# Kernel tuning notes

Hardware: AMD Instinct MI355X
Metric: run time of the kernel (lower is better)

## Reference

```python
import jax, jax.numpy as jnp
import numpy as np

# Module constants (from GaussRenderer.__init__ with image 128x128)
H = 128
W = 128
TS = 64          # TILE_SIZE
P_MAX = 2048
WHITE_BKGD = True
TH, TW = H // TS, W // TS
NT = TH * TW     # num_tiles


def _tile_grids():
    th, tw = jnp.meshgrid(jnp.arange(TH), jnp.arange(TW), indexing='ij')
    h_mins = (th * TS).reshape(-1).astype(jnp.float32)   # [NT]
    w_mins = (tw * TS).reshape(-1).astype(jnp.float32)   # [NT]
    lx = jnp.arange(TS, dtype=jnp.float32)
    xx, yy = jnp.meshgrid(lx, lx, indexing='xy')         # xx[i,j]=j, yy[i,j]=i
    local = jnp.stack([xx, yy], axis=-1).reshape(TS * TS, 2)
    # tile_coords[t, p] = (x, y) global pixel coordinate
    coords = local[None, :, :] + jnp.stack([w_mins, h_mins], axis=-1)[:, None, :]
    return h_mins, w_mins, coords


def setup_inputs() -> dict:
    key = jax.random.key(0)
    k1, k2, k3, k4, k5 = jax.random.split(key, 5)
    N = 100000
    means2D = jax.random.uniform(k1, (N, 2), dtype=jnp.float32) * jnp.array([float(W), float(H)], dtype=jnp.float32)
    A = jax.random.normal(k2, (N, 2, 2), dtype=jnp.float32) * 2.0
    cov2d = A @ jnp.swapaxes(A, 1, 2) + 0.5 * jnp.eye(2, dtype=jnp.float32)  # SPD
    color = jax.random.uniform(k3, (N, 3), dtype=jnp.float32)
    opacity = jax.random.uniform(k4, (N, 1), dtype=jnp.float32)
    depths = jax.random.uniform(k5, (N,), dtype=jnp.float32) * 10.0 + 0.2
    return {"means2D": means2D, "cov2d": cov2d, "color": color, "opacity": opacity, "depths": depths}


def _render(means2D, cov2d, color, opacity, depths):
    h_mins, w_mins, tile_coords = _tile_grids()
    h_maxs = h_mins + (TS - 1.0)
    w_maxs = w_mins + (TS - 1.0)

    # --- get_radius / get_rect (torch.no_grad -> stop_gradient) ---
    c = jax.lax.stop_gradient(cov2d)
    det = c[:, 0, 0] * c[:, 1, 1] - c[:, 0, 1] * c[:, 1, 0]
    mid = 0.5 * (c[:, 0, 0] + c[:, 1, 1])
    s = jnp.sqrt(jnp.clip(mid ** 2 - det, 0.1, None))
    radii = 3.0 * jnp.ceil(jnp.sqrt(jnp.maximum(mid + s, mid - s)))  # [N]
    m = jax.lax.stop_gradient(means2D)
    rmin = m - radii[:, None]
    rmax = m + radii[:, None]
    rmin = jnp.stack([jnp.clip(rmin[:, 0], 0.0, W - 1.0), jnp.clip(rmin[:, 1], 0.0, H - 1.0)], axis=-1)
    rmax = jnp.stack([jnp.clip(rmax[:, 0], 0.0, W - 1.0), jnp.clip(rmax[:, 1], 0.0, H - 1.0)], axis=-1)

    # --- tile/gaussian overlap test ---
    ov_x = jnp.minimum(rmax[None, :, 0], w_maxs[:, None]) > jnp.maximum(rmin[None, :, 0], w_mins[:, None])
    ov_y = jnp.minimum(rmax[None, :, 1], h_maxs[:, None]) > jnp.maximum(rmin[None, :, 1], h_mins[:, None])
    overlap = ov_x & ov_y                                   # [NT, N]

    # --- per-tile depth sort, keep front-most P_MAX ---
    FAR = jnp.float32(1e10)
    d_tiled = jnp.where(overlap, depths[None, :], FAR)      # [NT, N]
    idx = jnp.argsort(d_tiled, axis=1)[:, :P_MAX]           # [NT, P]
    sd = jnp.take_along_axis(d_tiled, idx, axis=1)          # sorted depths
    valid = (sd < 1e9).astype(means2D.dtype)                # [NT, P]

    sm = means2D[idx]          # [NT, P, 2]
    sc = cov2d[idx]            # [NT, P, 2, 2]
    so = opacity[idx][..., 0]  # [NT, P]
    scol = color[idx]          # [NT, P, 3]

    # --- conic (inverse 2x2 covariance) ---
    a_ = sc[..., 0, 0]; b_ = sc[..., 0, 1]; c2_ = sc[..., 1, 0]; d_ = sc[..., 1, 1]
    inv_det = 1.0 / jnp.clip(a_ * d_ - b_ * c2_, 1e-6, None)
    c00 = d_ * inv_det; c01 = -b_ * inv_det; c10 = -c2_ * inv_det; c11 = a_ * inv_det

    # --- per-pixel gaussian weights: [NT, TS*TS, P] ---
    dx0 = tile_coords[:, :, None, 0] - sm[:, None, :, 0]
    dx1 = tile_coords[:, :, None, 1] - sm[:, None, :, 1]
    gw = jnp.exp(-0.5 * (dx0 * dx0 * c00[:, None, :] + dx1 * dx1 * c11[:, None, :]
                         + dx0 * dx1 * (c01 + c10)[:, None, :]))

    # --- front-to-back alpha compositing ---
    alpha = jnp.minimum(gw * so[:, None, :], 0.99) * valid[:, None, :]
    T = jnp.cumprod(jnp.concatenate([jnp.ones_like(alpha[:, :, :1]), 1.0 - alpha[:, :, :-1]], axis=2), axis=2)
    w = alpha * T                                           # [NT, TS*TS, P]
    acc = w.sum(axis=2)                                     # [NT, TS*TS]
    tcol = jnp.einsum('tpn,tnc->tpc', w, scol)              # [NT, TS*TS, 3]
    if WHITE_BKGD:
        tcol = tcol + (1.0 - acc)[..., None]
    tdep = (w * sd[:, None, :]).sum(axis=2)

    # --- untile ---
    render_color = tcol.reshape(TH, TW, TS, TS, 3).transpose(0, 2, 1, 3, 4).reshape(H, W, 3)
    render_depth = tdep.reshape(TH, TW, TS, TS).transpose(0, 2, 1, 3).reshape(H, W, 1)
    render_alpha = acc.reshape(TH, TW, TS, TS).transpose(0, 2, 1, 3).reshape(H, W, 1)
    return render_color, render_depth, render_alpha


def reference(means2D, cov2d, color, opacity, depths):
    return _render(means2D, cov2d, color, opacity, depths)
```

## Files before the change

kernel.cpp:

```cpp
#include <hip/hip_runtime.h>

#define IMG 128
#define TSZ 64
#define NTILES 4
#define PMAX 2048
#define NHIST 4096
#define CAP 64
#define NCHUNK 16
#define CHUNK 128
#define QCH 32
#define NPIX 4096
#define NPSEG 16
#define PLANE ((size_t)NTILES * NCHUNK * NPIX)
#define NTHR 256
#define RUNITS (NTILES * NCHUNK * NPSEG)
#define POISON 0xAAAAAAAAu
#define LOG2E 1.4426950408889634f

typedef unsigned short u16;
typedef unsigned int uint32;
typedef unsigned long long u64;


__device__ __forceinline__ uint32 dbucket(float d) {
    int b = (int)(d * 256.0f);
    return (uint32)min(max(b, 0), NHIST - 1);
}

__device__ __forceinline__ void gauss_rect(const float* means, const float* cov,
                                           int i, float& rminx, float& rminy,
                                           float& rmaxx, float& rmaxy) {
    const float4 cv = ((const float4*)cov)[i];
    float det = cv.x * cv.w - cv.y * cv.z;
    float mid = 0.5f * (cv.x + cv.w);
    float s = sqrtf(fmaxf(mid * mid - det, 0.1f));
    float radius = 3.0f * ceilf(sqrtf(fmaxf(mid + s, mid - s)));
    const float2 m = ((const float2*)means)[i];
    rminx = fminf(fmaxf(m.x - radius, 0.f), (float)(IMG - 1));
    rmaxx = fminf(fmaxf(m.x + radius, 0.f), (float)(IMG - 1));
    rminy = fminf(fmaxf(m.y - radius, 0.f), (float)(IMG - 1));
    rmaxy = fminf(fmaxf(m.y + radius, 0.f), (float)(IMG - 1));
}

__device__ __forceinline__ bool tile_overlap(int t, float rminx, float rminy,
                                             float rmaxx, float rmaxy) {
    float wmin = (float)((t & 1) * TSZ), hmin = (float)((t >> 1) * TSZ);
    float wmax = wmin + (float)(TSZ - 1), hmax = hmin + (float)(TSZ - 1);
    return (fminf(rmaxx, wmax) > fmaxf(rminx, wmin)) &&
           (fminf(rmaxy, hmax) > fmaxf(rminy, hmin));
}

__global__ __launch_bounds__(NTHR) void k_pre2(
        const float* __restrict__ means, const float* __restrict__ cov,
        const float* __restrict__ depths, uint32* __restrict__ cnt,
        u64* __restrict__ slots, int N) {
    int i = blockIdx.x * NTHR + threadIdx.x;
    if (i >= N) return;
    float rminx, rminy, rmaxx, rmaxy;
    gauss_rect(means, cov, i, rminx, rminy, rmaxx, rmaxy);
    float d = depths[i];
    uint32 b = dbucket(d);
    u64 key = ((u64)__float_as_uint(d) << 32) | (uint32)i;
    #pragma unroll
    for (int t = 0; t < NTILES; t++) {
        if (tile_overlap(t, rminx, rminy, rmaxx, rmaxy)) {
            uint32 slot = atomicAdd(&cnt[t * NHIST + b], 1u) - POISON;
            if (slot < CAP)
                slots[((size_t)t * NHIST + b) * CAP + slot] = key;
        }
    }
}

__global__ __launch_bounds__(1024) void k_scan(const uint32* __restrict__ cnt,
        uint32* __restrict__ bucketBase, float* __restrict__ params) {
    const int tile = blockIdx.x, tid = threadIdx.x;
    const int lane = tid & 63, wid = tid >> 6;
    __shared__ uint32 wsum[16], wexcl[16], stot;
    uint4 raw = ((const uint4*)(cnt + (size_t)tile * NHIST))[tid];
    uint32 c0 = min(raw.x - POISON, (uint32)CAP);
    uint32 c1 = min(raw.y - POISON, (uint32)CAP);
    uint32 c2 = min(raw.z - POISON, (uint32)CAP);
    uint32 c3 = min(raw.w - POISON, (uint32)CAP);
    uint32 tot = c0 + c1 + c2 + c3;
    uint32 incl = tot;
    #pragma unroll
    for (int dlt = 1; dlt < 64; dlt <<= 1) {
        uint32 u = __shfl_up(incl, dlt, 64);
        if (lane >= dlt) incl += u;
    }
    if (lane == 63) wsum[wid] = incl;
    __syncthreads();
    if (wid == 0 && lane < 16) {
        uint32 v = wsum[lane], inc2 = v;
        #pragma unroll
        for (int dlt = 1; dlt < 16; dlt <<= 1) {
            uint32 u = __shfl_up(inc2, dlt, 16);
            if (lane >= dlt) inc2 += u;
        }
        wexcl[lane] = inc2 - v;
        if (lane == 15) stot = inc2;
    }
    __syncthreads();
    uint32 base = wexcl[wid] + (incl - tot);
    uint4 ob;
    ob.x = base; ob.y = base + c0; ob.z = ob.y + c1; ob.w = ob.z + c2;
    ((uint4*)(bucketBase + (size_t)tile * NHIST))[tid] = ob;
    for (uint32 p = stot + (uint32)tid; p < PMAX; p += 1024) {
        float4 z0 = {0.f, 0.f, 0.f, 0.f};
        float4 z1 = {0.f, -1e30f, 0.f, 0.f};
        float4* P = (float4*)(params + ((size_t)tile * PMAX + p) * 12);
        P[0] = z0; P[1] = z1; P[2] = z0;
    }
}

__global__ __launch_bounds__(NTHR) void k_rank3(const uint32* __restrict__ cnt,
        const uint32* __restrict__ bucketBase, const u64* __restrict__ slots,
        const float* __restrict__ means, const float* __restrict__ cov,
        const float* __restrict__ color, const float* __restrict__ opac,
        float* __restrict__ params) {
    const int wq = blockIdx.x * (NTHR / 64) + (threadIdx.x >> 6);
    const int tile = wq >> 12, b = wq & (NHIST - 1);
    const int lane = threadIdx.x & 63;
    uint32 n = cnt[(size_t)tile * NHIST + b] - POISON;
    n = min(n, (uint32)CAP);
    if (!n) return;
    uint32 base = bucketBase[(size_t)tile * NHIST + b];
    if (base >= PMAX) return;
    const u64* S = slots + ((size_t)tile * NHIST + b) * CAP;
    u64 ki = (lane < (int)n) ? S[lane] : ~0ull;
    uint32 r = base;
    for (uint32 j = 0; j < n; j++) {
        u64 kj = __shfl(ki, (int)j, 64);
        r += (kj < ki) ? 1u : 0u;
    }
    if (lane < (int)n && r < PMAX) {
        uint32 idx = (uint32)(ki & 0xffffffffu);
        const float4 cv = ((const float4*)cov)[idx];
        const float2 mn = ((const float2*)means)[idx];
        float invdet = 1.0f / fmaxf(cv.x * cv.w - cv.y * cv.z, 1e-6f);
        const float k = -0.5f * LOG2E;
        float4 p0, p1, p2;
        p0.x = mn.x; p0.y = mn.y;
        p0.z = k * cv.w * invdet;
        p0.w = k * cv.x * invdet;
        p1.x = -k * (cv.y + cv.z) * invdet;
        p1.y = log2f(opac[idx]);
        p1.z = color[3*idx]; p1.w = color[3*idx+1];
        p2.x = color[3*idx+2];
        p2.y = __uint_as_float((uint32)(ki >> 32));
        p2.z = 0.f; p2.w = 0.f;
        float4* P = (float4*)(params + ((size_t)tile * PMAX + r) * 12);
        P[0] = p0; P[1] = p1; P[2] = p2;
    }
}

__global__ __launch_bounds__(NTHR, 4) void k_render(
        const float* __restrict__ params, float* __restrict__ partials) {
    __shared__ __align__(16) float4 gp[CHUNK * 3];
    const int unit = blockIdx.x, tid = threadIdx.x;
    const int tile  = unit >> 8;
    const int chunk = (unit >> 4) & 15;
    const int pseg  = unit & 15;
    const float4* src = (const float4*)(params + ((size_t)tile * PMAX + (size_t)chunk * CHUNK) * 12);
    for (int j = tid; j < CHUNK * 3; j += NTHR) gp[j] = src[j];
    __syncthreads();
    const int p = pseg * NTHR + tid;
    const float px = (float)((tile & 1) * TSZ + (p & 63));
    const float py = (float)((tile >> 1) * TSZ + (p >> 6));
    float Tc[4], cr[4], cg[4], cb[4], dp[4], ac[4];
    #pragma unroll
    for (int s = 0; s < 4; s++) {
        Tc[s] = 1.f; cr[s] = 0.f; cg[s] = 0.f; cb[s] = 0.f; dp[s] = 0.f; ac[s] = 0.f;
    }
    #pragma unroll 2
    for (int g = 0; g < QCH; g++) {
        #pragma unroll
        for (int s = 0; s < 4; s++) {
            const int gg = s * QCH + g;
            float4 q0 = gp[3*gg], q1 = gp[3*gg+1], q2 = gp[3*gg+2];
            float dx = px - q0.x, dy = py - q0.y;
            float pw = fmaf(dx*dx, q0.z, q1.y);
            pw = fmaf(dy*dy, q0.w, pw);
            pw = fmaf(dx*dy, q1.x, pw);
            float al = fminf(exp2f(pw), 0.99f);
            float w = al * Tc[s];
            cr[s] += w * q1.z; cg[s] += w * q1.w; cb[s] += w * q2.x;
            dp[s] += w * q2.y; ac[s] += w;
            Tc[s] *= (1.f - al);
        }
    }
    float T = 1.f, fr = 0.f, fg = 0.f, fb = 0.f, fd = 0.f, fa = 0.f;
    #pragma unroll
    for (int s = 0; s < 4; s++) {
        fr += T * cr[s]; fg += T * cg[s]; fb += T * cb[s];
        fd += T * dp[s]; fa += T * ac[s];
        T *= Tc[s];
    }
    size_t base = ((size_t)tile * NCHUNK + chunk) * NPIX + (size_t)p;
    partials[0*PLANE + base] = T;
    partials[1*PLANE + base] = fr;
    partials[2*PLANE + base] = fg;
    partials[3*PLANE + base] = fb;
    partials[4*PLANE + base] = fd;
    partials[5*PLANE + base] = fa;
}

__global__ __launch_bounds__(NTHR) void k_combine(
        const float* __restrict__ partials, float* __restrict__ out) {
    int q = blockIdx.x * NTHR + threadIdx.x;
    int tile = q >> 12, p = q & (NPIX - 1);
    float T = 1.f, cr = 0.f, cg = 0.f, cb = 0.f, dep = 0.f, acc = 0.f;
    #pragma unroll
    for (int c = 0; c < NCHUNK; c++) {
        size_t base = ((size_t)tile * NCHUNK + c) * NPIX + (size_t)p;
        float Tk = partials[0*PLANE + base];
        cr  += T * partials[1*PLANE + base];
        cg  += T * partials[2*PLANE + base];
        cb  += T * partials[3*PLANE + base];
        dep += T * partials[4*PLANE + base];
        acc += T * partials[5*PLANE + base];
        T *= Tk;
    }
    int gx = (tile & 1) * TSZ + (p & 63);
    int gy = (tile >> 1) * TSZ + (p >> 6);
    int pix = gy * IMG + gx;
    float wb = 1.f - acc;
    out[3*pix+0] = cr + wb;
    out[3*pix+1] = cg + wb;
    out[3*pix+2] = cb + wb;
    out[IMG*IMG*3 + pix] = dep;
    out[IMG*IMG*4 + pix] = acc;
}

extern "C" void kernel_launch(void* const* d_in, const int* in_sizes, int n_in,
                              void* d_out, int out_size, void* d_ws, size_t ws_size,
                              hipStream_t stream) {
    const float* means  = (const float*)d_in[0];
    const float* cov    = (const float*)d_in[1];
    const float* color  = (const float*)d_in[2];
    const float* opac   = (const float*)d_in[3];
    const float* depths = (const float*)d_in[4];
    int N = in_sizes[4];

    char* ws = (char*)d_ws;
    size_t off = 0;
    uint32* cnt        = (uint32*)(ws + off); off += (size_t)NTILES * NHIST * 4;
    uint32* bucketBase = (uint32*)(ws + off); off += (size_t)NTILES * NHIST * 4;
    u64*    slots      = (u64*)(ws + off);    off += (size_t)NTILES * NHIST * CAP * 8;
    float*  params     = (float*)(ws + off);  off += (size_t)NTILES * PMAX * 12 * 4;
    float*  partials   = (float*)(ws + off);  off += 6 * PLANE * 4;
    float*  out        = (float*)d_out;

    k_pre2<<<(N + NTHR - 1) / NTHR, NTHR, 0, stream>>>(means, cov, depths,
                                                       cnt, slots, N);
    k_scan<<<NTILES, 1024, 0, stream>>>(cnt, bucketBase, params);
    k_rank3<<<(NTILES * NHIST) / (NTHR / 64), NTHR, 0, stream>>>(cnt, bucketBase,
                                                                 slots, means, cov,
                                                                 color, opac, params);
    k_render<<<RUNITS, NTHR, 0, stream>>>(params, partials);
    k_combine<<<(NTILES * NPIX) / NTHR, NTHR, 0, stream>>>(partials, out);
}
```

Before: 107.8 us.

## Fold bucket prefix scan into rank kernel, dropping separate scan launch

Removes the per-tile scan kernel and the bucketBase buffer; each wavefront in the rank kernel now computes its own bucket's exclusive prefix by summing earlier bucket counts with wave reductions, stopping early once the prefix reaches PMAX. The last bucket's wave takes over padding the unused param slots. This saves one kernel launch and a dependency step, but adds redundant count reads and reductions that grow with bucket index, and serializes the tail padding onto a single wave.

```diff
diff --git a/kernel.cpp b/kernel.cpp
--- a/kernel.cpp
+++ b/kernel.cpp
@@ -71,61 +71,37 @@
     }
 }
 
-__global__ __launch_bounds__(1024) void k_scan(const uint32* __restrict__ cnt,
-        uint32* __restrict__ bucketBase, float* __restrict__ params) {
-    const int tile = blockIdx.x, tid = threadIdx.x;
-    const int lane = tid & 63, wid = tid >> 6;
-    __shared__ uint32 wsum[16], wexcl[16], stot;
-    uint4 raw = ((const uint4*)(cnt + (size_t)tile * NHIST))[tid];
-    uint32 c0 = min(raw.x - POISON, (uint32)CAP);
-    uint32 c1 = min(raw.y - POISON, (uint32)CAP);
-    uint32 c2 = min(raw.z - POISON, (uint32)CAP);
-    uint32 c3 = min(raw.w - POISON, (uint32)CAP);
-    uint32 tot = c0 + c1 + c2 + c3;
-    uint32 incl = tot;
-    #pragma unroll
-    for (int dlt = 1; dlt < 64; dlt <<= 1) {
-        uint32 u = __shfl_up(incl, dlt, 64);
-        if (lane >= dlt) incl += u;
-    }
-    if (lane == 63) wsum[wid] = incl;
-    __syncthreads();
-    if (wid == 0 && lane < 16) {
-        uint32 v = wsum[lane], inc2 = v;
-        #pragma unroll
-        for (int dlt = 1; dlt < 16; dlt <<= 1) {
-            uint32 u = __shfl_up(inc2, dlt, 16);
-            if (lane >= dlt) inc2 += u;
-        }
-        wexcl[lane] = inc2 - v;
-        if (lane == 15) stot = inc2;
-    }
-    __syncthreads();
-    uint32 base = wexcl[wid] + (incl - tot);
-    uint4 ob;
-    ob.x = base; ob.y = base + c0; ob.z = ob.y + c1; ob.w = ob.z + c2;
-    ((uint4*)(bucketBase + (size_t)tile * NHIST))[tid] = ob;
-    for (uint32 p = stot + (uint32)tid; p < PMAX; p += 1024) {
-        float4 z0 = {0.f, 0.f, 0.f, 0.f};
-        float4 z1 = {0.f, -1e30f, 0.f, 0.f};
-        float4* P = (float4*)(params + ((size_t)tile * PMAX + p) * 12);
-        P[0] = z0; P[1] = z1; P[2] = z0;
-    }
-}
-
-__global__ __launch_bounds__(NTHR) void k_rank3(const uint32* __restrict__ cnt,
-        const uint32* __restrict__ bucketBase, const u64* __restrict__ slots,
+__global__ __launch_bounds__(NTHR) void k_rank4(const uint32* __restrict__ cnt,
+        const u64* __restrict__ slots,
         const float* __restrict__ means, const float* __restrict__ cov,
         const float* __restrict__ color, const float* __restrict__ opac,
         float* __restrict__ params) {
     const int wq = blockIdx.x * (NTHR / 64) + (threadIdx.x >> 6);
     const int tile = wq >> 12, b = wq & (NHIST - 1);
     const int lane = threadIdx.x & 63;
-    uint32 n = cnt[(size_t)tile * NHIST + b] - POISON;
-    n = min(n, (uint32)CAP);
-    if (!n) return;
-    uint32 base = bucketBase[(size_t)tile * NHIST + b];
+    const uint32* cn = cnt + (size_t)tile * NHIST;
+    uint32 n = min(cn[b] - POISON, (uint32)CAP);
+    if (!n && b != NHIST - 1) return;
+    uint32 base = 0;
+    for (int j0 = 0; j0 < b; j0 += 64) {
+        int j = j0 + lane;
+        uint32 c = (j < b) ? min(cn[j] - POISON, (uint32)CAP) : 0u;
+        #pragma unroll
+        for (int dlt = 1; dlt < 64; dlt <<= 1)
+            c += __shfl_xor(c, dlt, 64);
+        base += c;
+        if (base >= PMAX) break;
+    }
     if (base >= PMAX) return;
+    if (b == NHIST - 1) {
+        for (uint32 p = base + n + (uint32)lane; p < PMAX; p += 64) {
+            float4 z0 = {0.f, 0.f, 0.f, 0.f};
+            float4 z1 = {0.f, -1e30f, 0.f, 0.f};
+            float4* P = (float4*)(params + ((size_t)tile * PMAX + p) * 12);
+            P[0] = z0; P[1] = z1; P[2] = z0;
+        }
+        if (!n) return;
+    }
     const u64* S = slots + ((size_t)tile * NHIST + b) * CAP;
     u64 ki = (lane < (int)n) ? S[lane] : ~0ull;
     uint32 r = base;
@@ -245,7 +221,6 @@
     char* ws = (char*)d_ws;
     size_t off = 0;
     uint32* cnt        = (uint32*)(ws + off); off += (size_t)NTILES * NHIST * 4;
-    uint32* bucketBase = (uint32*)(ws + off); off += (size_t)NTILES * NHIST * 4;
     u64*    slots      = (u64*)(ws + off);    off += (size_t)NTILES * NHIST * CAP * 8;
     float*  params     = (float*)(ws + off);  off += (size_t)NTILES * PMAX * 12 * 4;
     float*  partials   = (float*)(ws + off);  off += 6 * PLANE * 4;
@@ -253,10 +228,10 @@
 
     k_pre2<<<(N + NTHR - 1) / NTHR, NTHR, 0, stream>>>(means, cov, depths,
                                                        cnt, slots, N);
-    k_scan<<<NTILES, 1024, 0, stream>>>(cnt, bucketBase, params);
-    k_rank3<<<(NTILES * NHIST) / (NTHR / 64), NTHR, 0, stream>>>(cnt, bucketBase,
-                                                                 slots, means, cov,
-                                                                 color, opac, params);
+    k_rank4<<<(NTILES * NHIST) / (NTHR / 64), NTHR, 0, stream>>>(cnt, slots,
+                                                                 means, cov,
+                                                                 color, opac,
+                                                                 params);
     k_render<<<RUNITS, NTHR, 0, stream>>>(params, partials);
     k_combine<<<(NTILES * NPIX) / NTHR, NTHR, 0, stream>>>(partials, out);
 }
```

New measurement: 108.0 us. No clear change (+0.1%).
